# Optimization experiments

Hardware: AMD Instinct MI355X
Metric: run time of the kernel (lower is better)

Reference implementation:

```python
import jax, jax.numpy as jnp
import numpy as np

# ---- cfg-derived constants (see init_kwargs) ----
AABB_MIN = np.array([-1.5, -1.5, -1.5], dtype=np.float32)
AABB_MAX = np.array([1.5, 1.5, 1.5], dtype=np.float32)
RES = np.array([128, 128, 128], dtype=np.int32)
NEAR = 2.0
FAR = 6.0
MAX_POINTS = 128
N_RAYS = 131072
CELL = (AABB_MAX - AABB_MIN) / RES.astype(np.float32)
STEP = float(0.5 * np.linalg.norm(CELL))  # half cell diagonal, as in _ray_match
MAX_STEPS = int(np.ceil((FAR - NEAR) / STEP)) + 2  # every ray terminates by then


def _ray_march(rays_o, rays_d, occ_grid):
    """Empty-space skipping: march each ray in STEP increments until it enters
    an occupied voxel (-> new_near = min(t, far)) or passes far (-> new_near = far)."""
    n = rays_o.shape[0]
    aabb_min = jnp.asarray(AABB_MIN)
    cell = jnp.asarray(CELL)
    res = jnp.asarray(RES)
    near = jnp.full((n,), NEAR, dtype=jnp.float32)
    far = jnp.full((n,), FAR, dtype=jnp.float32)

    def body(i, state):
        t, new_near, active = state
        t_next = t + STEP
        pts = rays_o + rays_d * t_next[:, None]            # (N, 3)
        # torch .long() truncates toward zero; int32 cast in jax matches that
        idx = ((pts - aabb_min) / cell).astype(jnp.int32)  # (N, 3)
        valid = jnp.all((idx >= 0) & (idx < res), axis=-1)
        ic = jnp.clip(idx, 0, res - 1)
        occ = occ_grid[ic[:, 0], ic[:, 1], ic[:, 2]]       # (N,) gather
        hit = active & valid & occ
        past = active & (t_next > far)
        miss = past & ~hit
        new_near = jnp.where(hit, jnp.minimum(t_next, far), new_near)
        new_near = jnp.where(miss, far, new_near)
        active = active & ~hit & ~past
        t = jnp.where(active, t_next, t)
        return (t, new_near, active)

    state0 = (near, near, jnp.ones((n,), dtype=bool))
    _, new_near, _ = jax.lax.fori_loop(0, MAX_STEPS, body, state0)
    return jnp.minimum(new_near, far)


def setup_inputs() -> dict:
    key = jax.random.key(0)
    k1, k2, k3 = jax.random.split(key, 3)
    origin = jnp.array([0.0, 0.0, 4.0], dtype=jnp.float32)
    rays_o = jnp.tile(origin, (N_RAYS, 1))
    # aim rays at random points inside the AABB so traversal is meaningful
    targets = jax.random.uniform(k1, (N_RAYS, 3), jnp.float32, -1.5, 1.5)
    d = targets - origin
    viewdirs = d / jnp.linalg.norm(d, axis=-1, keepdims=True)
    occ_grid = jax.random.uniform(k2, (128, 128, 128), jnp.float32) < 0.05
    t_rand = jax.random.uniform(k3, (N_RAYS, MAX_POINTS), jnp.float32)
    return {"rays_o": rays_o, "viewdirs": viewdirs, "t_rand": t_rand,
            "occ_grid": occ_grid}


def reference(rays_o, viewdirs, t_rand, occ_grid):
    # _ray_match runs under torch.no_grad() -> stop_gradient
    eff_near = jax.lax.stop_gradient(_ray_march(rays_o, viewdirs, occ_grid))
    t_vals = jnp.linspace(0.0, 1.0, MAX_POINTS, dtype=jnp.float32)
    z_vals = eff_near[:, None] * (1.0 - t_vals) + FAR * t_vals  # (N, S)
    # stratified perturbation (is_training and perturb > 0)
    mids = 0.5 * (z_vals[..., 1:] + z_vals[..., :-1])
    upper = jnp.concatenate([mids, z_vals[..., -1:]], axis=-1)
    lower = jnp.concatenate([z_vals[..., :1], mids], axis=-1)
    z_vals = lower + (upper - lower) * t_rand
    pts = rays_o[:, None, :] + viewdirs[:, None, :] * z_vals[..., None]  # (N, S, 3)
    return pts, z_vals
```

## Files before the change

kernel.cpp:

```cpp
#include <hip/hip_runtime.h>
#include <math.h>

#define NPTS      128
#define NEARV     2.0f
#define FARV      6.0f
#define GRID_RES  128
#define CELLV     0.0234375f

__global__ void init_flag_kernel(int* flag) { *flag = 0; }

__global__ void detect_layout_kernel(const unsigned int* __restrict__ g,
                                     int nwords, int* __restrict__ flag) {
    int i = blockIdx.x * blockDim.x + threadIdx.x;
    int stride = gridDim.x * blockDim.x;
    int local = 0;
    for (; i < nwords; i += stride)
        if (g[i] > 1u) local = 1;
    if (__any(local) && (threadIdx.x & 63) == 0)
        atomicOr(flag, 1);
}

__global__ void march_kernel(const float* __restrict__ rays_o,
                             const float* __restrict__ dirs,
                             const void*  __restrict__ grid,
                             const int*   __restrict__ flag,
                             float* __restrict__ eff_near,
                             int n, float step, int max_steps) {
    int r = blockIdx.x * blockDim.x + threadIdx.x;
    if (r >= n) return;

    const bool byte_layout = (*flag != 0);
    const unsigned char* gb = (const unsigned char*)grid;
    const int*           gi = (const int*)grid;

    float ox = rays_o[3 * r + 0], oy = rays_o[3 * r + 1], oz = rays_o[3 * r + 2];
    float dx = dirs[3 * r + 0],   dy = dirs[3 * r + 1],   dz = dirs[3 * r + 2];

    float t  = NEARV;
    float nn = NEARV;

    for (int i = 0; i < max_steps; ++i) {
        float tn = __fadd_rn(t, step);

        float px = __fadd_rn(ox, __fmul_rn(dx, tn));
        float py = __fadd_rn(oy, __fmul_rn(dy, tn));
        float pz = __fadd_rn(oz, __fmul_rn(dz, tn));

        float fx = __fdiv_rn(__fsub_rn(px, -1.5f), CELLV);
        float fy = __fdiv_rn(__fsub_rn(py, -1.5f), CELLV);
        float fz = __fdiv_rn(__fsub_rn(pz, -1.5f), CELLV);

        int ix = (int)fx;
        int iy = (int)fy;
        int iz = (int)fz;

        bool valid = (ix >= 0) & (ix < GRID_RES) &
                     (iy >= 0) & (iy < GRID_RES) &
                     (iz >= 0) & (iz < GRID_RES);

        bool occ = false;
        if (valid) {
            int cx = min(max(ix, 0), GRID_RES - 1);
            int cy = min(max(iy, 0), GRID_RES - 1);
            int cz = min(max(iz, 0), GRID_RES - 1);
            int lin = (cx << 14) | (cy << 7) | cz;
            occ = byte_layout ? (gb[lin] != 0) : (gi[lin] != 0);
        }

        bool hit  = occ;
        bool past = tn > FARV;

        if (hit)       nn = fminf(tn, FARV);
        else if (past) nn = FARV;

        if (hit | past) break;
        t = tn;
    }

    eff_near[r] = fminf(nn, FARV);
}

__device__ __forceinline__ float tval(int i) {
    const float delta = 1.0f / 127.0f;
    return (i >= NPTS - 1) ? 1.0f : __fmul_rn((float)i, delta);
}

__global__ void sample_kernel(const float* __restrict__ rays_o,
                              const float* __restrict__ dirs,
                              const float* __restrict__ t_rand,
                              const float* __restrict__ eff_near,
                              float* __restrict__ out_pts,
                              float* __restrict__ out_z,
                              int n) {
    int gid = blockIdx.x * blockDim.x + threadIdx.x;
    if (gid >= n * NPTS) return;
    int r = gid >> 7;
    int p = gid & (NPTS - 1);

    float en = eff_near[r];

    float tp = tval(p);
    float zp = __fadd_rn(__fmul_rn(en, __fsub_rn(1.0f, tp)), __fmul_rn(FARV, tp));

    float lower, upper;
    if (p == 0) {
        lower = zp;
    } else {
        float tm = tval(p - 1);
        float zm = __fadd_rn(__fmul_rn(en, __fsub_rn(1.0f, tm)), __fmul_rn(FARV, tm));
        lower = __fmul_rn(0.5f, __fadd_rn(zp, zm));
    }
    if (p == NPTS - 1) {
        upper = zp;
    } else {
        float tq = tval(p + 1);
        float zq = __fadd_rn(__fmul_rn(en, __fsub_rn(1.0f, tq)), __fmul_rn(FARV, tq));
        upper = __fmul_rn(0.5f, __fadd_rn(zp, zq));
    }

    float rr = t_rand[gid];
    float z  = __fadd_rn(lower, __fmul_rn(__fsub_rn(upper, lower), rr));

    out_z[gid] = z;

    float ox = rays_o[3 * r + 0], oy = rays_o[3 * r + 1], oz = rays_o[3 * r + 2];
    float dx = dirs[3 * r + 0],   dy = dirs[3 * r + 1],   dz = dirs[3 * r + 2];

    int b = gid * 3;
    out_pts[b + 0] = __fadd_rn(ox, __fmul_rn(dx, z));
    out_pts[b + 1] = __fadd_rn(oy, __fmul_rn(dy, z));
    out_pts[b + 2] = __fadd_rn(oz, __fmul_rn(dz, z));
}

extern "C" void kernel_launch(void* const* d_in, const int* in_sizes, int n_in,
                              void* d_out, int out_size, void* d_ws, size_t ws_size,
                              hipStream_t stream) {
    const float* rays_o = (const float*)d_in[0];
    const float* dirs   = (const float*)d_in[1];
    const float* t_rand = (const float*)d_in[2];
    const void*  occ    = d_in[3];

    int n    = in_sizes[0] / 3;
    int nocc = in_sizes[3];

    float* out     = (float*)d_out;
    float* out_pts = out;
    float* out_z   = out + (size_t)n * NPTS * 3;

    int*   flag = (int*)d_ws;
    float* eff  = (float*)((char*)d_ws + 256);

    float cell = CELLV;
    float step = 0.5f * sqrtf(3.0f * (cell * cell));
    int max_steps = (int)ceil((6.0 - 2.0) / (double)step) + 2;

    hipLaunchKernelGGL(init_flag_kernel, dim3(1), dim3(1), 0, stream, flag);
    hipLaunchKernelGGL(detect_layout_kernel, dim3(256), dim3(256), 0, stream,
                       (const unsigned int*)occ, nocc / 4, flag);
    hipLaunchKernelGGL(march_kernel, dim3((n + 255) / 256), dim3(256), 0, stream,
                       rays_o, dirs, occ, flag, eff, n, step, max_steps);

    long long total = (long long)n * NPTS;
    hipLaunchKernelGGL(sample_kernel, dim3((int)((total + 255) / 256)), dim3(256), 0, stream,
                       rays_o, dirs, t_rand, eff, out_pts, out_z, n);
}
```

Baseline: 439.2 us.

## Skip march to AABB entry, batch grid loads, vectorize sample stores

The march kernel now intersects each ray with the grid's bounding box and starts stepping just before the entry point, ending early past the exit. Step positions come from a shared-memory table, and four steps are evaluated per iteration so their grid loads can be issued together. The sample kernel handles four samples per thread, using 16-byte nontemporal loads and stores. The flag init kernel is replaced by a memset and the detect kernel uses more blocks. The entry/exit estimate and the few-step slack must exactly match the reference's per-step rounding, otherwise edge rays could give different results.

```diff
diff --git a/kernel.cpp b/kernel.cpp
--- a/kernel.cpp
+++ b/kernel.cpp
@@ -6,8 +6,9 @@
 #define FARV      6.0f
 #define GRID_RES  128
 #define CELLV     0.0234375f
-
-__global__ void init_flag_kernel(int* flag) { *flag = 0; }
+#define TSZ       256
+
+typedef float f4 __attribute__((ext_vector_type(4)));
 
 __global__ void detect_layout_kernel(const unsigned int* __restrict__ g,
                                      int nwords, int* __restrict__ flag) {
@@ -20,61 +21,90 @@
         atomicOr(flag, 1);
 }
 
-__global__ void march_kernel(const float* __restrict__ rays_o,
-                             const float* __restrict__ dirs,
-                             const void*  __restrict__ grid,
-                             const int*   __restrict__ flag,
-                             float* __restrict__ eff_near,
-                             int n, float step, int max_steps) {
-    int r = blockIdx.x * blockDim.x + threadIdx.x;
+__global__ __launch_bounds__(256) void march_kernel(
+        const float* __restrict__ rays_o,
+        const float* __restrict__ dirs,
+        const unsigned char* __restrict__ grid,
+        const int* __restrict__ flag,
+        float* __restrict__ eff_near,
+        int n, float step, int max_steps) {
+    __shared__ float T[TSZ];
+    int tid = threadIdx.x;
+    if (tid <= max_steps) {
+        float t = NEARV;
+        for (int k = 0; k < tid; ++k) t = __fadd_rn(t, step);
+        T[tid] = t;
+    } else if (tid < TSZ) {
+        T[tid] = 1.0e9f;
+    }
+    __syncthreads();
+
+    int r = blockIdx.x * blockDim.x + tid;
     if (r >= n) return;
 
-    const bool byte_layout = (*flag != 0);
-    const unsigned char* gb = (const unsigned char*)grid;
-    const int*           gi = (const int*)grid;
+    const int shift = (*flag != 0) ? 0 : 2;
 
     float ox = rays_o[3 * r + 0], oy = rays_o[3 * r + 1], oz = rays_o[3 * r + 2];
     float dx = dirs[3 * r + 0],   dy = dirs[3 * r + 1],   dz = dirs[3 * r + 2];
 
-    float t  = NEARV;
+    const float BMIN = -1.5f - CELLV;
+    float t1x = (BMIN - ox) / dx, t2x = (1.5f - ox) / dx;
+    float t1y = (BMIN - oy) / dy, t2y = (1.5f - oy) / dy;
+    float t1z = (BMIN - oz) / dz, t2z = (1.5f - oz) / dz;
+    float tent = fmaxf(fmaxf(fminf(t1x, t2x), fminf(t1y, t2y)),
+                       fmaxf(fminf(t1z, t2z), NEARV));
+    float texi = fminf(fminf(fmaxf(t1x, t2x), fmaxf(t1y, t2y)),
+                       fminf(fmaxf(t1z, t2z), FARV));
+
     float nn = NEARV;
-
-    for (int i = 0; i < max_steps; ++i) {
-        float tn = __fadd_rn(t, step);
-
-        float px = __fadd_rn(ox, __fmul_rn(dx, tn));
-        float py = __fadd_rn(oy, __fmul_rn(dy, tn));
-        float pz = __fadd_rn(oz, __fmul_rn(dz, tn));
-
-        float fx = __fdiv_rn(__fsub_rn(px, -1.5f), CELLV);
-        float fy = __fdiv_rn(__fsub_rn(py, -1.5f), CELLV);
-        float fz = __fdiv_rn(__fsub_rn(pz, -1.5f), CELLV);
-
-        int ix = (int)fx;
-        int iy = (int)fy;
-        int iz = (int)fz;
-
-        bool valid = (ix >= 0) & (ix < GRID_RES) &
-                     (iy >= 0) & (iy < GRID_RES) &
-                     (iz >= 0) & (iz < GRID_RES);
-
-        bool occ = false;
-        if (valid) {
-            int cx = min(max(ix, 0), GRID_RES - 1);
-            int cy = min(max(iy, 0), GRID_RES - 1);
-            int cz = min(max(iz, 0), GRID_RES - 1);
-            int lin = (cx << 14) | (cy << 7) | cz;
-            occ = byte_layout ? (gb[lin] != 0) : (gi[lin] != 0);
+    if (!(tent <= texi)) {
+        nn = FARV;
+    } else {
+        int i0 = (int)floorf((tent - NEARV) / step) - 3;
+        if (i0 < 0) i0 = 0;
+        float texm = texi + 3.0f * step;
+        bool done = false;
+        for (int i = i0; i < max_steps && !done; i += 4) {
+            float tn[4];
+            int   lin[4];
+            bool  val[4];
+#pragma unroll
+            for (int j = 0; j < 4; ++j) {
+                float t_n = T[i + 1 + j];
+                tn[j] = t_n;
+                float px = __fadd_rn(ox, __fmul_rn(dx, t_n));
+                float py = __fadd_rn(oy, __fmul_rn(dy, t_n));
+                float pz = __fadd_rn(oz, __fmul_rn(dz, t_n));
+                float fx = __fdiv_rn(__fsub_rn(px, -1.5f), CELLV);
+                float fy = __fdiv_rn(__fsub_rn(py, -1.5f), CELLV);
+                float fz = __fdiv_rn(__fsub_rn(pz, -1.5f), CELLV);
+                int ix = (int)fx;
+                int iy = (int)fy;
+                int iz = (int)fz;
+                val[j] = ((unsigned)ix < (unsigned)GRID_RES) &
+                         ((unsigned)iy < (unsigned)GRID_RES) &
+                         ((unsigned)iz < (unsigned)GRID_RES);
+                int cx = min(max(ix, 0), GRID_RES - 1);
+                int cy = min(max(iy, 0), GRID_RES - 1);
+                int cz = min(max(iz, 0), GRID_RES - 1);
+                lin[j] = (cx << 14) | (cy << 7) | cz;
+            }
+            unsigned char oc[4];
+#pragma unroll
+            for (int j = 0; j < 4; ++j)
+                oc[j] = grid[(size_t)((unsigned)lin[j]) << shift];
+            for (int j = 0; j < 4 && !done; ++j) {
+                bool hit  = val[j] && (oc[j] != 0);
+                bool past = tn[j] > FARV;
+                if (hit)       { nn = fminf(tn[j], FARV); done = true; }
+                else if (past) { nn = FARV;               done = true; }
+            }
+            if (!done && T[i + 5] > texm) {
+                nn = FARV;
+                done = true;
+            }
         }
-
-        bool hit  = occ;
-        bool past = tn > FARV;
-
-        if (hit)       nn = fminf(tn, FARV);
-        else if (past) nn = FARV;
-
-        if (hit | past) break;
-        t = tn;
+        if (!done) nn = fminf(nn, FARV);
     }
 
     eff_near[r] = fminf(nn, FARV);
@@ -85,51 +115,67 @@
     return (i >= NPTS - 1) ? 1.0f : __fmul_rn((float)i, delta);
 }
 
-__global__ void sample_kernel(const float* __restrict__ rays_o,
-                              const float* __restrict__ dirs,
-                              const float* __restrict__ t_rand,
-                              const float* __restrict__ eff_near,
-                              float* __restrict__ out_pts,
-                              float* __restrict__ out_z,
-                              int n) {
+__device__ __forceinline__ float zmid(float en, int i) {
+    float ti = tval(i);
+    return __fadd_rn(__fmul_rn(en, __fsub_rn(1.0f, ti)), __fmul_rn(FARV, ti));
+}
+
+__global__ __launch_bounds__(256) void sample_kernel(
+        const float* __restrict__ rays_o,
+        const float* __restrict__ dirs,
+        const float* __restrict__ t_rand,
+        const float* __restrict__ eff_near,
+        float* __restrict__ out_pts,
+        float* __restrict__ out_z,
+        int n) {
     int gid = blockIdx.x * blockDim.x + threadIdx.x;
-    if (gid >= n * NPTS) return;
-    int r = gid >> 7;
-    int p = gid & (NPTS - 1);
+    if (gid >= n * (NPTS / 4)) return;
+    int r  = gid >> 5;
+    int p0 = (gid & 31) << 2;
 
     float en = eff_near[r];
-
-    float tp = tval(p);
-    float zp = __fadd_rn(__fmul_rn(en, __fsub_rn(1.0f, tp)), __fmul_rn(FARV, tp));
-
-    float lower, upper;
-    if (p == 0) {
-        lower = zp;
-    } else {
-        float tm = tval(p - 1);
-        float zm = __fadd_rn(__fmul_rn(en, __fsub_rn(1.0f, tm)), __fmul_rn(FARV, tm));
-        lower = __fmul_rn(0.5f, __fadd_rn(zp, zm));
-    }
-    if (p == NPTS - 1) {
-        upper = zp;
-    } else {
-        float tq = tval(p + 1);
-        float zq = __fadd_rn(__fmul_rn(en, __fsub_rn(1.0f, tq)), __fmul_rn(FARV, tq));
-        upper = __fmul_rn(0.5f, __fadd_rn(zp, zq));
-    }
-
-    float rr = t_rand[gid];
-    float z  = __fadd_rn(lower, __fmul_rn(__fsub_rn(upper, lower), rr));
-
-    out_z[gid] = z;
+    f4 rr = __builtin_nontemporal_load(((const f4*)t_rand) + gid);
+
+    float z[4];
+#pragma unroll
+    for (int j = 0; j < 4; ++j) {
+        int p = p0 + j;
+        float zp = zmid(en, p);
+        float lower, upper;
+        if (p == 0) {
+            lower = zp;
+        } else {
+            lower = __fmul_rn(0.5f, __fadd_rn(zp, zmid(en, p - 1)));
+        }
+        if (p == NPTS - 1) {
+            upper = zp;
+        } else {
+            upper = __fmul_rn(0.5f, __fadd_rn(zp, zmid(en, p + 1)));
+        }
+        z[j] = __fadd_rn(lower, __fmul_rn(__fsub_rn(upper, lower), rr[j]));
+    }
+
+    f4 zv = { z[0], z[1], z[2], z[3] };
+    __builtin_nontemporal_store(zv, ((f4*)out_z) + gid);
 
     float ox = rays_o[3 * r + 0], oy = rays_o[3 * r + 1], oz = rays_o[3 * r + 2];
     float dx = dirs[3 * r + 0],   dy = dirs[3 * r + 1],   dz = dirs[3 * r + 2];
 
-    int b = gid * 3;
-    out_pts[b + 0] = __fadd_rn(ox, __fmul_rn(dx, z));
-    out_pts[b + 1] = __fadd_rn(oy, __fmul_rn(dy, z));
-    out_pts[b + 2] = __fadd_rn(oz, __fmul_rn(dz, z));
+    float X[4], Y[4], Z[4];
+#pragma unroll
+    for (int j = 0; j < 4; ++j) {
+        X[j] = __fadd_rn(ox, __fmul_rn(dx, z[j]));
+        Y[j] = __fadd_rn(oy, __fmul_rn(dy, z[j]));
+        Z[j] = __fadd_rn(oz, __fmul_rn(dz, z[j]));
+    }
+
+    f4 a = { X[0], Y[0], Z[0], X[1] };
+    f4 b = { Y[1], Z[1], X[2], Y[2] };
+    f4 c = { Z[2], X[3], Y[3], Z[3] };
+    f4* pdst = ((f4*)out_pts) + (size_t)gid * 3;
+    __builtin_nontemporal_store(a, pdst + 0);
+    __builtin_nontemporal_store(b, pdst + 1);
+    __builtin_nontemporal_store(c, pdst + 2);
 }
 
 extern "C" void kernel_launch(void* const* d_in, const int* in_sizes, int n_in,
@@ -154,13 +200,13 @@
     float step = 0.5f * sqrtf(3.0f * (cell * cell));
     int max_steps = (int)ceil((6.0 - 2.0) / (double)step) + 2;
 
-    hipLaunchKernelGGL(init_flag_kernel, dim3(1), dim3(1), 0, stream, flag);
-    hipLaunchKernelGGL(detect_layout_kernel, dim3(256), dim3(256), 0, stream,
+    hipMemsetAsync(flag, 0, sizeof(int), stream);
+    hipLaunchKernelGGL(detect_layout_kernel, dim3(512), dim3(256), 0, stream,
                        (const unsigned int*)occ, nocc / 4, flag);
     hipLaunchKernelGGL(march_kernel, dim3((n + 255) / 256), dim3(256), 0, stream,
-                       rays_o, dirs, occ, flag, eff, n, step, max_steps);
-
-    long long total = (long long)n * NPTS;
-    hipLaunchKernelGGL(sample_kernel, dim3((int)((total + 255) / 256)), dim3(256), 0, stream,
+                       rays_o, dirs, (const unsigned char*)occ, flag, eff, n, step, max_steps);
+
+    int total4 = n * (NPTS / 4);
+    hipLaunchKernelGGL(sample_kernel, dim3((total4 + 255) / 256), dim3(256), 0, stream,
                        rays_o, dirs, t_rand, eff, out_pts, out_z, n);
 }
```

New measurement: 461.7 us. 5.1% more time.
